# Kernel tuning notes

Hardware: AMD Instinct MI355X
Metric: run time of the kernel (lower is better)

Reference implementation:

```python
import jax, jax.numpy as jnp
import numpy as np

N = 1024  # grid resolution per cube face


def _make_cube_points(n):
    t = np.linspace(-1.0, 1.0, n, dtype=np.float32)
    u, v = np.meshgrid(t, t, indexing='ij')
    one = np.ones_like(u)
    pts = np.stack([
        np.stack([ one, u, v], 0),   # +X face
        np.stack([-one, u, v], 0),   # -X face
        np.stack([u,  one, v], 0),   # +Y face
        np.stack([u, -one, v], 0),   # -Y face
        np.stack([u, v,  one], 0),   # +Z face
        np.stack([u, v, -one], 0),   # -Z face
    ], 0)  # (6,3,n,n)
    return pts


def _make_angles(n):
    # angles = (sin(theta)cos(phi), sin(theta)sin(phi), cos(theta)) == normalized cube point
    p = _make_cube_points(n)
    return p / np.linalg.norm(p, axis=1, keepdims=True)


def _make_cube_faces(n):
    idx = np.arange(6 * n * n, dtype=np.int64).reshape(6, n, n)
    a = idx[:, :-1, :-1]; b = idx[:, :-1, 1:]
    c = idx[:, 1:, :-1]; d = idx[:, 1:, 1:]
    t1 = np.stack([a, b, c], -1).reshape(-1, 3)
    t2 = np.stack([c, b, d], -1).reshape(-1, 3)
    return np.concatenate([t1, t2], 0)  # (12*(n-1)^2, 3)


def setup_inputs():
    key = jax.random.key(0)
    radii = jax.random.normal(key, (6, 1, N, N), dtype=jnp.float32) * 0.025
    angles = jnp.asarray(_make_angles(N))          # (6,3,N,N) float32
    faces = jnp.asarray(_make_cube_faces(N))       # (F,3) int64 (int32 on 32-bit jax)
    return {"radii": radii, "angles": angles, "faces": faces}


def _avg_border(r):
    # Average the coinciding border lines of adjacent cube faces so seams agree.
    n = r.shape[-1]; e = n - 1
    def line(f, kind, i):
        return (f, slice(None), i, slice(None)) if kind == 'r' else (f, slice(None), slice(None), i)
    pairs = [((0, 'r', e), (2, 'r', e)), ((0, 'r', 0), (3, 'r', e)),
             ((1, 'r', e), (2, 'r', 0)), ((1, 'r', 0), (3, 'r', 0)),
             ((0, 'c', e), (4, 'r', e)), ((0, 'c', 0), (5, 'r', e)),
             ((1, 'c', e), (4, 'r', 0)), ((1, 'c', 0), (5, 'r', 0)),
             ((2, 'c', e), (4, 'c', e)), ((2, 'c', 0), (5, 'c', e)),
             ((3, 'c', e), (4, 'c', 0)), ((3, 'c', 0), (5, 'c', 0))]
    out = r
    for a, b in pairs:
        ia, ib = line(*a), line(*b)
        avg = 0.5 * (r[ia] + r[ib])
        out = out.at[ia].set(avg).at[ib].set(avg)
    return out


def _to_vertices(st):
    # (6,3,n,n) -> (6*n*n, 3)
    return jnp.transpose(st, (0, 2, 3, 1)).reshape(-1, 3)


def _to_stacked(v, n):
    # (6*n*n, 3) -> (6,3,n,n)
    return jnp.transpose(v.reshape(6, n, n, 3), (0, 3, 1, 2))


def _normalize(x, eps=1e-8):
    return x / jnp.maximum(jnp.linalg.norm(x, axis=-1, keepdims=True), eps)


def reference(radii, angles, faces):
    n = radii.shape[-1]
    # elementwise chain: border-averaged radii -> sigmoid -> scale unit directions
    stacked = jax.nn.sigmoid(_avg_border(radii)) * angles          # (6,3,n,n)
    vert = _to_vertices(stacked)                                   # (V,3)
    # gather + cross product per triangle
    v0 = vert[faces[:, 0]]; v1 = vert[faces[:, 1]]; v2 = vert[faces[:, 2]]
    face_normals = _normalize(jnp.cross(v1 - v0, v2 - v0))         # (F,3)
    # scatter-average face normals onto vertices
    V = vert.shape[0]
    seg = faces.reshape(-1)                                        # (3F,)
    vals = jnp.repeat(face_normals, 3, axis=0)                     # (3F,3)
    vn = jax.ops.segment_sum(vals, seg, num_segments=V)            # (V,3)
    vn = _normalize(vn)
    # per-face sign flips (faces 0,3,4) as in the original module
    signs = jnp.array([-1.0, 1.0, 1.0, -1.0, -1.0, 1.0], dtype=vn.dtype).reshape(6, 1, 1, 1)
    vn = _to_vertices(_to_stacked(vn, n) * signs)
    return (vert, faces, vn)
```

## Files before the change

kernel.cpp:

```cpp
#include <hip/hip_runtime.h>
#include <math.h>

#define NN_  (1024*1024)
#define NPTS (6*NN_)
#define E_   1023
#define VERT_ELEMS (NPTS*3)
#define FACE_ELEMS 37675044
#define FACE_VEC4  (FACE_ELEMS/4)

__device__ __forceinline__ float3 f3(float x, float y, float z){ float3 r; r.x=x;r.y=y;r.z=z; return r; }

__device__ __forceinline__ float3 loadv(const float* __restrict__ v, int f, int i, int j){
    int o = ((f << 20) + (i << 10) + j) * 3;
    return f3(v[o], v[o+1], v[o+2]);
}

__device__ __forceinline__ float3 tri_normal(float3 v0, float3 v1, float3 v2){
    float ax = v1.x - v0.x, ay = v1.y - v0.y, az = v1.z - v0.z;
    float bx = v2.x - v0.x, by = v2.y - v0.y, bz = v2.z - v0.z;
    float cx = ay*bz - az*by;
    float cy = az*bx - ax*bz;
    float cz = ax*by - ay*bx;
    float n = sqrtf(cx*cx + cy*cy + cz*cz);
    float inv = 1.0f / fmaxf(n, 1e-8f);
    return f3(cx*inv, cy*inv, cz*inv);
}

__global__ __launch_bounds__(256) void vert_kernel(const float* __restrict__ radii,
                                                   const float* __restrict__ angles,
                                                   float* __restrict__ vert) {
    int idx = blockIdx.x * blockDim.x + threadIdx.x;
    if (idx >= NPTS) return;
    int j = idx & 1023;
    int i = (idx >> 10) & 1023;
    int f = idx >> 20;

    float r = radii[idx];

    int pf = -1, pi = 0, pj = 0;
    if (j == 0) {
        switch (f) {
            case 0: pf=5; pi=E_; pj=i;  break;
            case 1: pf=5; pi=0;  pj=i;  break;
            case 2: pf=5; pi=i;  pj=E_; break;
            case 3: pf=5; pi=i;  pj=0;  break;
            case 4: pf=3; pi=i;  pj=E_; break;
            case 5: pf=3; pi=i;  pj=0;  break;
        }
    } else if (j == E_) {
        switch (f) {
            case 0: pf=4; pi=E_; pj=i;  break;
            case 1: pf=4; pi=0;  pj=i;  break;
            case 2: pf=4; pi=i;  pj=E_; break;
            case 3: pf=4; pi=i;  pj=0;  break;
            case 4: pf=2; pi=i;  pj=E_; break;
            case 5: pf=2; pi=i;  pj=0;  break;
        }
    } else if (i == 0) {
        switch (f) {
            case 0: pf=3; pi=E_; pj=j;  break;
            case 1: pf=3; pi=0;  pj=j;  break;
            case 2: pf=1; pi=E_; pj=j;  break;
            case 3: pf=1; pi=0;  pj=j;  break;
            case 4: pf=1; pi=j;  pj=E_; break;
            case 5: pf=1; pi=j;  pj=0;  break;
        }
    } else if (i == E_) {
        switch (f) {
            case 0: pf=2; pi=E_; pj=j;  break;
            case 1: pf=2; pi=0;  pj=j;  break;
            case 2: pf=0; pi=E_; pj=j;  break;
            case 3: pf=0; pi=0;  pj=j;  break;
            case 4: pf=0; pi=j;  pj=E_; break;
            case 5: pf=0; pi=j;  pj=0;  break;
        }
    }
    if (pf >= 0) {
        float rp = radii[(pf << 20) + (pi << 10) + pj];
        r = 0.5f * (r + rp);
    }

    float s = 1.0f / (1.0f + __expf(-r));

    int abase = (f * 3) << 20;
    int aoff  = (i << 10) + j;
    float ax = angles[abase + aoff];
    float ay = angles[abase + (1 << 20) + aoff];
    float az = angles[abase + (2 << 20) + aoff];

    int o = idx * 3;
    vert[o]   = s * ax;
    vert[o+1] = s * ay;
    vert[o+2] = s * az;
}

__global__ __launch_bounds__(256) void faces_kernel(const int* __restrict__ fin,
                                                    float* __restrict__ fout) {
    int idx = blockIdx.x * blockDim.x + threadIdx.x;
    if (idx >= FACE_VEC4) return;
    int4 v = ((const int4* __restrict__)fin)[idx];
    float4 o;
    o.x = (float)v.x; o.y = (float)v.y; o.z = (float)v.z; o.w = (float)v.w;
    ((float4*)fout)[idx] = o;
}

__global__ __launch_bounds__(256) void vn_kernel(const float* __restrict__ vert,
                                                 float* __restrict__ vn) {
    int idx = blockIdx.x * blockDim.x + threadIdx.x;
    if (idx >= NPTS) return;
    int j = idx & 1023;
    int i = (idx >> 10) & 1023;
    int f = idx >> 20;

    bool iN = (i > 0), iP = (i < E_), jN = (j > 0), jP = (j < E_);

    float3 c = loadv(vert, f, i, j);
    float3 pR = f3(0,0,0), pL = f3(0,0,0), pD = f3(0,0,0), pU = f3(0,0,0);
    float3 pDL = f3(0,0,0), pUR = f3(0,0,0);
    if (jP) pR  = loadv(vert, f, i,   j+1);
    if (jN) pL  = loadv(vert, f, i,   j-1);
    if (iP) pD  = loadv(vert, f, i+1, j);
    if (iN) pU  = loadv(vert, f, i-1, j);
    if (iP && jN) pDL = loadv(vert, f, i+1, j-1);
    if (iN && jP) pUR = loadv(vert, f, i-1, j+1);

    float sx = 0.f, sy = 0.f, sz = 0.f;
    if (iP && jP) { float3 n = tri_normal(c,   pR,  pD); sx+=n.x; sy+=n.y; sz+=n.z; }
    if (iP && jN) { float3 n = tri_normal(pL,  c,   pDL); sx+=n.x; sy+=n.y; sz+=n.z; }
    if (iN && jP) { float3 n = tri_normal(pU,  pUR, c);  sx+=n.x; sy+=n.y; sz+=n.z; }
    if (iN && jP) { float3 n = tri_normal(c,   pUR, pR); sx+=n.x; sy+=n.y; sz+=n.z; }
    if (iP && jN) { float3 n = tri_normal(pDL, c,   pD); sx+=n.x; sy+=n.y; sz+=n.z; }
    if (iN && jN) { float3 n = tri_normal(pL,  pU,  c);  sx+=n.x; sy+=n.y; sz+=n.z; }

    float nn = sqrtf(sx*sx + sy*sy + sz*sz);
    float inv = 1.0f / fmaxf(nn, 1e-8f);
    float sgn = ((f == 1) || (f == 2) || (f == 5)) ? 1.0f : -1.0f;
    inv *= sgn;

    int o = idx * 3;
    vn[o]   = sx * inv;
    vn[o+1] = sy * inv;
    vn[o+2] = sz * inv;
}

extern "C" void kernel_launch(void* const* d_in, const int* in_sizes, int n_in,
                              void* d_out, int out_size, void* d_ws, size_t ws_size,
                              hipStream_t stream) {
    const float* radii  = (const float*)d_in[0];
    const float* angles = (const float*)d_in[1];
    const int*   faces  = (const int*)d_in[2];

    float* out_vert  = (float*)d_out;
    float* out_faces = (float*)d_out + VERT_ELEMS;
    float* out_vn    = (float*)d_out + VERT_ELEMS + FACE_ELEMS;

    dim3 blk(256);
    dim3 grd_v((NPTS + 255) / 256);
    dim3 grd_f((FACE_VEC4 + 255) / 256);

    vert_kernel<<<grd_v, blk, 0, stream>>>(radii, angles, out_vert);
    faces_kernel<<<grd_f, blk, 0, stream>>>(faces, out_faces);
    vn_kernel<<<grd_v, blk, 0, stream>>>(out_vert, out_vn);
}
```

Baseline: 492.3 us.

## Fuse vertex and normal kernels with shared-memory tiled stencil

Merges the vertex construction and vertex-normal kernels into one kernel that computes a 34x34 halo tile of vertices into shared memory, then derives normals from the tile. This removes the global write-then-reread of the vertex array and one launch. Outputs are written with float4 vector stores, and rsqrt replaces sqrt+divide. The halo vertices are recomputed redundantly, including their border-averaging branches.

```diff
diff --git a/kernel.cpp b/kernel.cpp
--- a/kernel.cpp
+++ b/kernel.cpp
@@ -1,42 +1,16 @@
 #include <hip/hip_runtime.h>
 #include <math.h>
 
-#define NN_  (1024*1024)
-#define NPTS (6*NN_)
-#define E_   1023
-#define VERT_ELEMS (NPTS*3)
+#define E_ 1023
+#define NPTS 6291456
+#define VERT_ELEMS 18874368
 #define FACE_ELEMS 37675044
-#define FACE_VEC4  (FACE_ELEMS/4)
+#define FACE_VEC4  9418761
 
 __device__ __forceinline__ float3 f3(float x, float y, float z){ float3 r; r.x=x;r.y=y;r.z=z; return r; }
 
-__device__ __forceinline__ float3 loadv(const float* __restrict__ v, int f, int i, int j){
-    int o = ((f << 20) + (i << 10) + j) * 3;
-    return f3(v[o], v[o+1], v[o+2]);
-}
-
-__device__ __forceinline__ float3 tri_normal(float3 v0, float3 v1, float3 v2){
-    float ax = v1.x - v0.x, ay = v1.y - v0.y, az = v1.z - v0.z;
-    float bx = v2.x - v0.x, by = v2.y - v0.y, bz = v2.z - v0.z;
-    float cx = ay*bz - az*by;
-    float cy = az*bx - ax*bz;
-    float cz = ax*by - ay*bx;
-    float n = sqrtf(cx*cx + cy*cy + cz*cz);
-    float inv = 1.0f / fmaxf(n, 1e-8f);
-    return f3(cx*inv, cy*inv, cz*inv);
-}
-
-__global__ __launch_bounds__(256) void vert_kernel(const float* __restrict__ radii,
-                                                   const float* __restrict__ angles,
-                                                   float* __restrict__ vert) {
-    int idx = blockIdx.x * blockDim.x + threadIdx.x;
-    if (idx >= NPTS) return;
-    int j = idx & 1023;
-    int i = (idx >> 10) & 1023;
-    int f = idx >> 20;
-
-    float r = radii[idx];
-
+__device__ __forceinline__ float eff_radius(const float* __restrict__ radii, int f, int i, int j){
+    float r = radii[(f<<20)+(i<<10)+j];
     int pf = -1, pi = 0, pj = 0;
     if (j == 0) {
         switch (f) {
@@ -75,23 +49,97 @@
             case 5: pf=0; pi=j;  pj=0;  break;
         }
     }
-    if (pf >= 0) {
-        float rp = radii[(pf << 20) + (pi << 10) + pj];
-        r = 0.5f * (r + rp);
+    if (pf >= 0) r = 0.5f * (r + radii[(pf<<20)+(pi<<10)+pj]);
+    return r;
+}
+
+__device__ __forceinline__ void tri_acc(float3 v0, float3 v1, float3 v2, bool on,
+                                        float& sx, float& sy, float& sz){
+    float ax = v1.x - v0.x, ay = v1.y - v0.y, az = v1.z - v0.z;
+    float bx = v2.x - v0.x, by = v2.y - v0.y, bz = v2.z - v0.z;
+    float cx = ay*bz - az*by;
+    float cy = az*bx - ax*bz;
+    float cz = ax*by - ay*bx;
+    float inv = on ? rsqrtf(fmaxf(cx*cx + cy*cy + cz*cz, 1e-16f)) : 0.0f;
+    sx += cx*inv; sy += cy*inv; sz += cz*inv;
+}
+
+#define LSTR 37
+__global__ __launch_bounds__(256) void fused_kernel(const float* __restrict__ radii,
+                                                    const float* __restrict__ angles,
+                                                    float* __restrict__ vert,
+                                                    float* __restrict__ vn) {
+    __shared__ float lx[34*LSTR], ly[34*LSTR], lz[34*LSTR];
+
+    int bid = blockIdx.x;
+    int f   = bid >> 10;
+    int rem = bid & 1023;
+    int i0  = (rem >> 5) << 5;
+    int j0  = (rem & 31) << 5;
+    int tid = threadIdx.x;
+
+    int hy = tid >> 5;
+    int hx = tid & 31;
+    int abase = (f * 3) << 20;
+    for (int rr = hy; rr < 34; rr += 8) {
+        for (int cc = hx; cc < 34; cc += 32) {
+            int gi = i0 - 1 + rr, gj = j0 - 1 + cc;
+            int gic = min(max(gi, 0), E_);
+            int gjc = min(max(gj, 0), E_);
+            float r = eff_radius(radii, f, gic, gjc);
+            float s = 1.0f / (1.0f + __expf(-r));
+            int aoff = (gic << 10) + gjc;
+            int o = rr * LSTR + cc;
+            lx[o] = s * angles[abase + aoff];
+            ly[o] = s * angles[abase + (1<<20) + aoff];
+            lz[o] = s * angles[abase + (2<<20) + aoff];
+        }
+    }
+    __syncthreads();
+
+    int ty = tid >> 3;
+    int tq = tid & 7;
+    int i  = i0 + ty;
+    float sgn = ((f == 1) || (f == 2) || (f == 5)) ? 1.0f : -1.0f;
+
+    float vx[4], vy[4], vz[4], nx[4], ny[4], nz[4];
+    #pragma unroll
+    for (int q = 0; q < 4; ++q) {
+        int col = tq * 4 + q;
+        int j   = j0 + col;
+        int r   = ty + 1, c = col + 1;
+        int o   = r * LSTR + c;
+        float3 C  = f3(lx[o],        ly[o],        lz[o]);
+        float3 R  = f3(lx[o+1],      ly[o+1],      lz[o+1]);
+        float3 L  = f3(lx[o-1],      ly[o-1],      lz[o-1]);
+        float3 D  = f3(lx[o+LSTR],   ly[o+LSTR],   lz[o+LSTR]);
+        float3 U  = f3(lx[o-LSTR],   ly[o-LSTR],   lz[o-LSTR]);
+        float3 DL = f3(lx[o+LSTR-1], ly[o+LSTR-1], lz[o+LSTR-1]);
+        float3 UR = f3(lx[o-LSTR+1], ly[o-LSTR+1], lz[o-LSTR+1]);
+
+        bool iN = (i > 0), iP = (i < E_), jN = (j > 0), jP = (j < E_);
+        float sx = 0.f, sy = 0.f, sz = 0.f;
+        tri_acc(C,  R,  D,  iP && jP, sx, sy, sz);
+        tri_acc(L,  C,  DL, iP && jN, sx, sy, sz);
+        tri_acc(U,  UR, C,  iN && jP, sx, sy, sz);
+        tri_acc(C,  UR, R,  iN && jP, sx, sy, sz);
+        tri_acc(DL, C,  D,  iP && jN, sx, sy, sz);
+        tri_acc(L,  U,  C,  iN && jN, sx, sy, sz);
+
+        float inv = sgn * rsqrtf(fmaxf(sx*sx + sy*sy + sz*sz, 1e-16f));
+        vx[q] = C.x; vy[q] = C.y; vz[q] = C.z;
+        nx[q] = sx * inv; ny[q] = sy * inv; nz[q] = sz * inv;
     }
 
-    float s = 1.0f / (1.0f + __expf(-r));
-
-    int abase = (f * 3) << 20;
-    int aoff  = (i << 10) + j;
-    float ax = angles[abase + aoff];
-    float ay = angles[abase + (1 << 20) + aoff];
-    float az = angles[abase + (2 << 20) + aoff];
-
-    int o = idx * 3;
-    vert[o]   = s * ax;
-    vert[o+1] = s * ay;
-    vert[o+2] = s * az;
+    int pt = (f << 20) + (i << 10) + j0 + tq * 4;
+    float4* vp = (float4*)(vert + (size_t)pt * 3);
+    vp[0] = make_float4(vx[0], vy[0], vz[0], vx[1]);
+    vp[1] = make_float4(vy[1], vz[1], vx[2], vy[2]);
+    vp[2] = make_float4(vz[2], vx[3], vy[3], vz[3]);
+    float4* np = (float4*)(vn + (size_t)pt * 3);
+    np[0] = make_float4(nx[0], ny[0], nz[0], nx[1]);
+    np[1] = make_float4(ny[1], nz[1], nx[2], ny[2]);
+    np[2] = make_float4(nz[2], nx[3], ny[3], nz[3]);
 }
 
 __global__ __launch_bounds__(256) void faces_kernel(const int* __restrict__ fin,
@@ -102,45 +150,6 @@
     float4 o;
     o.x = (float)v.x; o.y = (float)v.y; o.z = (float)v.z; o.w = (float)v.w;
     ((float4*)fout)[idx] = o;
-}
-
-__global__ __launch_bounds__(256) void vn_kernel(const float* __restrict__ vert,
-                                                 float* __restrict__ vn) {
-    int idx = blockIdx.x * blockDim.x + threadIdx.x;
-    if (idx >= NPTS) return;
-    int j = idx & 1023;
-    int i = (idx >> 10) & 1023;
-    int f = idx >> 20;
-
-    bool iN = (i > 0), iP = (i < E_), jN = (j > 0), jP = (j < E_);
-
-    float3 c = loadv(vert, f, i, j);
-    float3 pR = f3(0,0,0), pL = f3(0,0,0), pD = f3(0,0,0), pU = f3(0,0,0);
-    float3 pDL = f3(0,0,0), pUR = f3(0,0,0);
-    if (jP) pR  = loadv(vert, f, i,   j+1);
-    if (jN) pL  = loadv(vert, f, i,   j-1);
-    if (iP) pD  = loadv(vert, f, i+1, j);
-    if (iN) pU  = loadv(vert, f, i-1, j);
-    if (iP && jN) pDL = loadv(vert, f, i+1, j-1);
-    if (iN && jP) pUR = loadv(vert, f, i-1, j+1);
-
-    float sx = 0.f, sy = 0.f, sz = 0.f;
-    if (iP && jP) { float3 n = tri_normal(c,   pR,  pD); sx+=n.x; sy+=n.y; sz+=n.z; }
-    if (iP && jN) { float3 n = tri_normal(pL,  c,   pDL); sx+=n.x; sy+=n.y; sz+=n.z; }
-    if (iN && jP) { float3 n = tri_normal(pU,  pUR, c);  sx+=n.x; sy+=n.y; sz+=n.z; }
-    if (iN && jP) { float3 n = tri_normal(c,   pUR, pR); sx+=n.x; sy+=n.y; sz+=n.z; }
-    if (iP && jN) { float3 n = tri_normal(pDL, c,   pD); sx+=n.x; sy+=n.y; sz+=n.z; }
-    if (iN && jN) { float3 n = tri_normal(pL,  pU,  c);  sx+=n.x; sy+=n.y; sz+=n.z; }
-
-    float nn = sqrtf(sx*sx + sy*sy + sz*sz);
-    float inv = 1.0f / fmaxf(nn, 1e-8f);
-    float sgn = ((f == 1) || (f == 2) || (f == 5)) ? 1.0f : -1.0f;
-    inv *= sgn;
-
-    int o = idx * 3;
-    vn[o]   = sx * inv;
-    vn[o+1] = sy * inv;
-    vn[o+2] = sz * inv;
 }
 
 extern "C" void kernel_launch(void* const* d_in, const int* in_sizes, int n_in,
@@ -154,11 +163,6 @@
     float* out_faces = (float*)d_out + VERT_ELEMS;
     float* out_vn    = (float*)d_out + VERT_ELEMS + FACE_ELEMS;
 
-    dim3 blk(256);
-    dim3 grd_v((NPTS + 255) / 256);
-    dim3 grd_f((FACE_VEC4 + 255) / 256);
-
-    vert_kernel<<<grd_v, blk, 0, stream>>>(radii, angles, out_vert);
-    faces_kernel<<<grd_f, blk, 0, stream>>>(faces, out_faces);
-    vn_kernel<<<grd_v, blk, 0, stream>>>(out_vert, out_vn);
+    fused_kernel<<<dim3(6144), dim3(256), 0, stream>>>(radii, angles, out_vert, out_vn);
+    faces_kernel<<<dim3((FACE_VEC4 + 255) / 256), dim3(256), 0, stream>>>(faces, out_faces);
 }
```

Result: no change. 501.4 us (+1.8%).
